# Kernel optimization log

Measured on AMD Instinct MI355X. Metric: run time of the kernel, lower is better.

The kernel has to match this reference:

```python
import jax, jax.numpy as jnp
import numpy as np

B, D, H, L = 2048, 4096, 1024, 64
LAM = 1.0  # topo_lambda


def setup_inputs() -> dict:
    key = jax.random.key(0)
    ks = jax.random.split(key, 5)
    def w(k, sh):
        fan_in = sh[0]
        return (jax.random.normal(k, sh, jnp.float32) * (1.0 / fan_in) ** 0.5)
    return {
        "x": jax.random.normal(ks[0], (B, D), jnp.float32),
        "W1": w(ks[1], (D, H)), "b1": jnp.zeros((H,), jnp.float32),
        "W2": w(ks[2], (H, L)), "b2": jnp.zeros((L,), jnp.float32),
        "W3": w(ks[3], (L, H)), "b3": jnp.zeros((H,), jnp.float32),
        "W4": w(ks[4], (H, D)), "b4": jnp.zeros((D,), jnp.float32),
        "latent_norm": jnp.ones((1,), jnp.float32),
    }


def _cdist(a):
    # pairwise euclidean distances [N, N], safe sqrt (zero grad on zero diag)
    sq = jnp.sum(a * a, axis=1)
    d2 = jnp.maximum(sq[:, None] + sq[None, :] - 2.0 * (a @ a.T), 0.0)
    pos = d2 > 0
    return jnp.where(pos, jnp.sqrt(jnp.where(pos, d2, 1.0)), 0.0)


def _mst_edges(d):
    # 0-dim persistence pairs == MST edges of the dense distance matrix.
    # Vectorized Prim's algorithm: scan of N-1 steps, O(N) work per step.
    n = d.shape[0]
    in_tree = jnp.zeros((n,), bool).at[0].set(True)
    min_dist = d[0]
    parent = jnp.zeros((n,), jnp.int32)

    def step(carry, _):
        in_tree, min_dist, parent = carry
        j = jnp.argmin(jnp.where(in_tree, jnp.inf, min_dist)).astype(jnp.int32)
        i = parent[j]
        in_tree = in_tree.at[j].set(True)
        better = (d[j] < min_dist) & ~in_tree
        min_dist = jnp.where(better, d[j], min_dist)
        parent = jnp.where(better, j, parent)
        return (in_tree, min_dist, parent), jnp.stack([i, j])

    _, edges = jax.lax.scan(step, (in_tree, min_dist, parent), None, length=n - 1)
    return edges  # [n-1, 2] int32


def _topo_signature(dx, dz):
    # pairing indices computed on detached distances (as in torch .detach())
    p1 = _mst_edges(jax.lax.stop_gradient(dx))
    p2 = _mst_edges(jax.lax.stop_gradient(dz))
    sig1 = dx[p1[:, 0], p1[:, 1]]
    sig1_2 = dz[p1[:, 0], p1[:, 1]]
    sig2 = dz[p2[:, 0], p2[:, 1]]
    sig2_1 = dx[p2[:, 0], p2[:, 1]]
    # match_edges == 'symmetric'
    return jnp.sum((sig1 - sig1_2) ** 2) + jnp.sum((sig2 - sig2_1) ** 2)


def reference(x, W1, b1, W2, b2, W3, b3, W4, b4, latent_norm):
    z = jax.nn.relu(x @ W1 + b1) @ W2 + b2            # [B, L]
    x_rec = jax.nn.relu(z @ W3 + b3) @ W4 + b4        # [B, D]
    rec_loss = jnp.mean((x_rec - x) ** 2)
    x_dist = _cdist(x)
    x_dist = x_dist / jnp.max(x_dist)
    z_dist = _cdist(z) / latent_norm[0]
    topo_loss = _topo_signature(x_dist, z_dist) / x.shape[0]
    loss = rec_loss + LAM * topo_loss
    return loss
```

## Files before the change

kernel.cpp:

```cpp
#include <hip/hip_runtime.h>
#include <hip/hip_bf16.h>

#define B_N 2048
#define D_N 4096
#define H_N 1024
#define L_N 64
#define NTILE 136
#define SPLK 4

typedef __attribute__((ext_vector_type(8))) short short8;
typedef __attribute__((ext_vector_type(4))) float float4_t;

#define ASG __attribute__((address_space(1)))
#define ASL __attribute__((address_space(3)))

__device__ inline float bf2f(unsigned short u) {
  union { unsigned u; float f; } v; v.u = ((unsigned)u) << 16; return v.f;
}
__device__ inline unsigned short f2bf(float f) {
  union { float f; unsigned u; } v; v.f = f;
  unsigned r = v.u + 0x7fffu + ((v.u >> 16) & 1u);
  return (unsigned short)(r >> 16);
}

__device__ inline float block_sum256(float v) {
  const int lane = threadIdx.x & 63, wave = threadIdx.x >> 6;
#pragma unroll
  for (int off = 32; off; off >>= 1) v += __shfl_xor(v, off);
  __shared__ float red_s[4];
  if (lane == 0) red_s[wave] = v;
  __syncthreads();
  return red_s[0] + red_s[1] + red_s[2] + red_s[3];
}

__device__ inline float block_max256(float v) {
  const int lane = threadIdx.x & 63, wave = threadIdx.x >> 6;
#pragma unroll
  for (int off = 32; off; off >>= 1) v = fmaxf(v, __shfl_xor(v, off));
  __shared__ float redm_s[4];
  if (lane == 0) redm_s[wave] = v;
  __syncthreads();
  return fmaxf(fmaxf(redm_s[0], redm_s[1]), fmaxf(redm_s[2], redm_s[3]));
}

__device__ inline void tri_idx(int b, int& tm, int& tn) {
  int m = (int)((sqrtf(8.f * (float)b + 1.f) - 1.f) * 0.5f);
  while ((m + 1) * (m + 2) / 2 <= b) ++m;
  while (m * (m + 1) / 2 > b) --m;
  tm = m;
  tn = b - m * (m + 1) / 2;
}

__global__ __launch_bounds__(256) void mega_prep(const float* __restrict__ x,
                                                 const float* __restrict__ W1,
                                                 const float* __restrict__ W4,
                                                 unsigned short* __restrict__ xb,
                                                 unsigned short* __restrict__ w1bt,
                                                 unsigned short* __restrict__ w4bt,
                                                 float* __restrict__ sqx,
                                                 float* __restrict__ accum,
                                                 int* __restrict__ comp,
                                                 unsigned long long* __restrict__ rowbest,
                                                 int* __restrict__ cnt,
                                                 int* __restrict__ done) {
  const int b = blockIdx.x;
  const int t = threadIdx.x;
  if (b < B_N) {
    const float4* xr = (const float4*)(x + (size_t)b * D_N);
    float s = 0.f;
    for (int i = t; i < D_N / 4; i += 256) {
      float4 v = xr[i];
      s += v.x * v.x + v.y * v.y + v.z * v.z + v.w * v.w;
      ushort4 o;
      o.x = f2bf(v.x); o.y = f2bf(v.y); o.z = f2bf(v.z); o.w = f2bf(v.w);
      const int p = i >> 3;
      const int k31 = (4 * i) & 31;
      *(ushort4*)(xb + ((size_t)p * B_N + b) * 32 + k31) = o;
    }
    float tot = block_sum256(s);
    if (t == 0) sqx[b] = tot;
    return;
  }
  if (b == B_N) {
    if (t < 2) { accum[t] = 0.f; cnt[t] = 0; done[t] = 0; }
    for (int v = t; v < 2 * B_N; v += 256) {
      comp[v] = v & (B_N - 1);
      rowbest[v] = ~0ull;
    }
    return;
  }
  int tb = b - (B_N + 1);
  const float* in;
  unsigned short* out;
  int C, bx, by;
  if (tb < 4096) { in = W1; out = w1bt; C = H_N; bx = tb & 31;  by = tb >> 5; }
  else { tb -= 4096; in = W4; out = w4bt; C = D_N; bx = tb & 127; by = tb >> 7; }
  const int c0 = bx * 32, r0 = by * 32;
  const int tx = t & 31, ty = t >> 5;
  __shared__ float tile[32][33];
#pragma unroll
  for (int i = 0; i < 32; i += 8)
    tile[ty + i][tx] = in[(size_t)(r0 + ty + i) * C + c0 + tx];
  __syncthreads();
#pragma unroll
  for (int i = 0; i < 32; i += 8)
    out[((size_t)(r0 >> 5) * C + c0 + ty + i) * 32 + tx] = f2bf(tile[tx][ty + i]);
}

__device__ inline void gemm_mainloop(const unsigned short* __restrict__ A,
                                     const unsigned short* __restrict__ Bt,
                                     int nrA, int nrB, int Klen, int m_base, int n_base,
                                     float4_t acc[4][4]) {
  __shared__ unsigned short lA[128 * 32];
  __shared__ unsigned short lB[128 * 32];
  const int t = threadIdx.x;
  const int wave = t >> 6;
  const int lane = t & 63;
  const int lrow = lane & 15;
  const int quad = lane >> 4;
  const int wm = (wave & 1) * 64;
  const int wn = (wave >> 1) * 64;
  const int srow = lane >> 2;
  const int scol = (lane & 3) * 8;

  for (int k0 = 0; k0 < Klen; k0 += 32) {
    const size_t pA = (size_t)(k0 >> 5) * nrA;
    const size_t pB = (size_t)(k0 >> 5) * nrB;
    __syncthreads();
#pragma unroll
    for (int q = 0; q < 2; ++q) {
      const int rbase = wave * 32 + q * 16;
      const int row = rbase + srow;
      __builtin_amdgcn_global_load_lds(
          (ASG void*)(A + (pA + m_base + row) * 32 + scol),
          (ASL void*)(lA + rbase * 32), 16, 0, 0);
      __builtin_amdgcn_global_load_lds(
          (ASG void*)(Bt + (pB + n_base + row) * 32 + scol),
          (ASL void*)(lB + rbase * 32), 16, 0, 0);
    }
    __syncthreads();
    short8 af[4], bfr[4];
#pragma unroll
    for (int f = 0; f < 4; ++f) {
      af[f]  = *(const short8*)(lA + (wm + f * 16 + lrow) * 32 + quad * 8);
      bfr[f] = *(const short8*)(lB + (wn + f * 16 + lrow) * 32 + quad * 8);
    }
#pragma unroll
    for (int fm = 0; fm < 4; ++fm)
#pragma unroll
      for (int fn = 0; fn < 4; ++fn)
        acc[fm][fn] = __builtin_amdgcn_mfma_f32_16x16x32_bf16(af[fm], bfr[fn],
                                                              acc[fm][fn], 0, 0, 0);
  }
}

__global__ __launch_bounds__(256) void mega_gemm(const unsigned short* __restrict__ xb,
                                                 const unsigned short* __restrict__ w1bt,
                                                 float* __restrict__ partsG1,
                                                 float* __restrict__ partsD2) {
  float4_t acc[4][4];
  float4_t z4 = {0.f, 0.f, 0.f, 0.f};
#pragma unroll
  for (int a = 0; a < 4; ++a)
#pragma unroll
    for (int b2 = 0; b2 < 4; ++b2) acc[a][b2] = z4;
  const int b = blockIdx.x;
  const int t = threadIdx.x, wave = t >> 6, lane = t & 63;
  const int lrow = lane & 15, quad = lane >> 4;
  const int wm = (wave & 1) * 64, wn = (wave >> 1) * 64;

  if (b < 512) {
    const int s = b >> 7;
    const int tt = b & 127;
    const int m_base = (tt >> 3) * 128, n_base = (tt & 7) * 128;
    const size_t po = (size_t)(s * 32);
    gemm_mainloop(xb + po * B_N * 32, w1bt + po * H_N * 32, B_N, H_N, D_N / SPLK,
                  m_base, n_base, acc);
    float* __restrict__ P = partsG1 + (size_t)s * B_N * H_N;
#pragma unroll
    for (int fm = 0; fm < 4; ++fm)
#pragma unroll
      for (int fn = 0; fn < 4; ++fn) {
        const int r0 = m_base + wm + fm * 16 + quad * 4;
        const int c = n_base + wn + fn * 16 + lrow;
#pragma unroll
        for (int r = 0; r < 4; ++r)
          P[(size_t)(r0 + r) * H_N + c] = acc[fm][fn][r];
      }
  } else {
    const int c = b - 512;
    const int s = c / NTILE;
    const int tt = c - s * NTILE;
    const int tile = (tt & 7) * 17 + (tt >> 3);
    int tm, tn;
    tri_idx(tile, tm, tn);
    const size_t po = (size_t)(s * 32) * B_N * 32;
    gemm_mainloop(xb + po, xb + po, B_N, B_N, D_N / SPLK, tm * 128, tn * 128, acc);
    float* __restrict__ P = partsD2 + ((size_t)s * NTILE + tile) * 16384;
#pragma unroll
    for (int fm = 0; fm < 4; ++fm)
#pragma unroll
      for (int fn = 0; fn < 4; ++fn) {
        const int lr0 = wm + fm * 16 + quad * 4;
        const int lc = wn + fn * 16 + lrow;
#pragma unroll
        for (int r = 0; r < 4; ++r)
          P[(lr0 + r) * 128 + lc] = acc[fm][fn][r];
      }
  }
}

__global__ __launch_bounds__(256) void mega_fin(const float* __restrict__ partsG1,
                                                const float* __restrict__ partsD2,
                                                const float* __restrict__ bias,
                                                const float* __restrict__ sq,
                                                unsigned short* __restrict__ h1b,
                                                float* __restrict__ d2x,
                                                unsigned* __restrict__ max_slot) {
  const int b = blockIdx.x;
  const int t = threadIdx.x;
  if (b < 2048) {
    const size_t MN = (size_t)B_N * H_N;
    const size_t i4 = ((size_t)b * 256 + t) * 4;
    float4 a = *(const float4*)(partsG1 + i4);
#pragma unroll
    for (int s = 1; s < SPLK; ++s) {
      float4 p = *(const float4*)(partsG1 + s * MN + i4);
      a.x += p.x; a.y += p.y; a.z += p.z; a.w += p.w;
    }
    const int row = (int)(i4 >> 10);
    const int k = (int)(i4 & (H_N - 1));
    float4 bb = *(const float4*)(bias + k);
    ushort4 o;
    o.x = f2bf(fmaxf(a.x + bb.x, 0.f));
    o.y = f2bf(fmaxf(a.y + bb.y, 0.f));
    o.z = f2bf(fmaxf(a.z + bb.z, 0.f));
    o.w = f2bf(fmaxf(a.w + bb.w, 0.f));
    *(ushort4*)(h1b + ((size_t)(k >> 5) * B_N + row) * 32 + (k & 31)) = o;
    return;
  }
  const int cidx = b - 2048;
  const int tile = cidx >> 2;
  const int c0 = (cidx & 3) * 32;
  int tm, tn;
  tri_idx(tile, tm, tn);
  __shared__ float lds[32][132];
  const int cc = (t & 7) * 4;
  float lmax = 0.f;
#pragma unroll
  for (int q = 0; q < 4; ++q) {
    const int r = (t >> 3) + 32 * q;
    const float* base = partsD2 + (size_t)tile * 16384 + r * 128 + c0 + cc;
    float4 a = *(const float4*)base;
#pragma unroll
    for (int s = 1; s < SPLK; ++s) {
      float4 p = *(const float4*)(base + (size_t)s * NTILE * 16384);
      a.x += p.x; a.y += p.y; a.z += p.z; a.w += p.w;
    }
    const int i = tm * 128 + r;
    const float si = sq[i];
    float4 sj = *(const float4*)(sq + tn * 128 + c0 + cc);
    float4 v;
    v.x = fmaxf(si + sj.x - 2.f * a.x, 0.f);
    v.y = fmaxf(si + sj.y - 2.f * a.y, 0.f);
    v.z = fmaxf(si + sj.z - 2.f * a.z, 0.f);
    v.w = fmaxf(si + sj.w - 2.f * a.w, 0.f);
    *(float4*)(d2x + (size_t)i * B_N + tn * 128 + c0 + cc) = v;
    lds[cc + 0][r] = v.x;
    lds[cc + 1][r] = v.y;
    lds[cc + 2][r] = v.z;
    lds[cc + 3][r] = v.w;
    lmax = fmaxf(lmax, fmaxf(fmaxf(v.x, v.y), fmaxf(v.z, v.w)));
  }
  __syncthreads();
#pragma unroll
  for (int m = 0; m < 4; ++m) {
    const int lin = t + 256 * m;
    const int cc2 = lin >> 5;
    const int r4 = (lin & 31) * 4;
    float4 w = *(const float4*)(&lds[cc2][r4]);
    *(float4*)(d2x + (size_t)(tn * 128 + c0 + cc2) * B_N + tm * 128 + r4) = w;
  }
  float tot = block_max256(lmax);
  if (t == 0) atomicMax(max_slot, __float_as_uint(tot));
}

__global__ __launch_bounds__(256) void g2_k(const unsigned short* __restrict__ h1b,
                                            const float* __restrict__ W2,
                                            const float* __restrict__ b2,
                                            float* __restrict__ z,
                                            float* __restrict__ sqz) {
  const int col = threadIdx.x & 63;
  const int row = blockIdx.x * 4 + (threadIdx.x >> 6);
  float a0 = 0.f, a1 = 0.f, a2 = 0.f, a3 = 0.f;
  for (int p = 0; p < H_N / 32; ++p) {
    const unsigned short* hb = h1b + ((size_t)p * B_N + row) * 32;
    const float* wb = W2 + (p * 32) * L_N + col;
#pragma unroll
    for (int k2 = 0; k2 < 32; k2 += 4) {
      a0 += bf2f(hb[k2 + 0]) * wb[(k2 + 0) * L_N];
      a1 += bf2f(hb[k2 + 1]) * wb[(k2 + 1) * L_N];
      a2 += bf2f(hb[k2 + 2]) * wb[(k2 + 2) * L_N];
      a3 += bf2f(hb[k2 + 3]) * wb[(k2 + 3) * L_N];
    }
  }
  const float zv = (a0 + a1) + (a2 + a3) + b2[col];
  z[(size_t)row * L_N + col] = zv;
  float s = zv * zv;
#pragma unroll
  for (int off = 32; off; off >>= 1) s += __shfl_xor(s, off);
  if (col == 0) sqz[row] = s;
}

__global__ __launch_bounds__(256) void mega_g3_d2z(const float* __restrict__ z,
                                                   const float* __restrict__ W3,
                                                   const float* __restrict__ b3,
                                                   const float* __restrict__ sqz,
                                                   unsigned short* __restrict__ h2b,
                                                   float* __restrict__ d2z) {
  const int b = blockIdx.x;
  const int t = threadIdx.x;
  if (b < 2048) {
    const int rg = b & 511, cg = b >> 9;
    const int col = cg * 256 + t;
    const int r0 = rg * 4;
    __shared__ float zr[4][64];
    zr[t >> 6][t & 63] = z[(size_t)(r0 + (t >> 6)) * L_N + (t & 63)];
    __syncthreads();
    const float bc = b3[col];
    float a0 = bc, a1 = bc, a2 = bc, a3 = bc;
#pragma unroll 8
    for (int k = 0; k < 64; ++k) {
      float w = W3[k * H_N + col];
      a0 += zr[0][k] * w;
      a1 += zr[1][k] * w;
      a2 += zr[2][k] * w;
      a3 += zr[3][k] * w;
    }
    const size_t base = ((size_t)(col >> 5) * B_N) * 32 + (col & 31);
    h2b[base + (size_t)(r0 + 0) * 32] = f2bf(fmaxf(a0, 0.f));
    h2b[base + (size_t)(r0 + 1) * 32] = f2bf(fmaxf(a1, 0.f));
    h2b[base + (size_t)(r0 + 2) * 32] = f2bf(fmaxf(a2, 0.f));
    h2b[base + (size_t)(r0 + 3) * 32] = f2bf(fmaxf(a3, 0.f));
    return;
  }
  const int c = b - 2048;
  const int bi = (c >> 7) * 16, bj = (c & 127) * 16;
  __shared__ float zi[16][65], zj[16][65];
  for (int idx = t; idx < 16 * 64; idx += 256) {
    const int r = idx >> 6, cc = idx & 63;
    zi[r][cc] = z[(size_t)(bi + r) * L_N + cc];
    zj[r][cc] = z[(size_t)(bj + r) * L_N + cc];
  }
  __syncthreads();
  const int ti = t >> 4, tj = t & 15;
  float dot = 0.f;
#pragma unroll 8
  for (int k = 0; k < 64; ++k) dot += zi[ti][k] * zj[tj][k];
  float v = fmaxf(sqz[bi + ti] + sqz[bj + tj] - 2.f * dot, 0.f);
  d2z[(size_t)(bi + ti) * B_N + bj + tj] = v;
}

__device__ inline void scan_row(const float* __restrict__ row, const int* __restrict__ cp,
                                int i, int ci, unsigned long long* __restrict__ dst) {
  const int t = threadIdx.x;
  const unsigned ibase = (unsigned)(i << 11);
  unsigned long long k = ~0ull;
#pragma unroll
  for (int m = 0; m < 2; ++m) {
    const int j4 = (t + m * 256) * 4;
    float4 dv = *(const float4*)(row + j4);
    int4 cj = *(const int4*)(cp + j4);
    if (cj.x != ci) {
      unsigned long long key = (((unsigned long long)__float_as_uint(dv.x)) << 32) | (ibase | (unsigned)(j4 + 0));
      k = key < k ? key : k;
    }
    if (cj.y != ci) {
      unsigned long long key = (((unsigned long long)__float_as_uint(dv.y)) << 32) | (ibase | (unsigned)(j4 + 1));
      k = key < k ? key : k;
    }
    if (cj.z != ci) {
      unsigned long long key = (((unsigned long long)__float_as_uint(dv.z)) << 32) | (ibase | (unsigned)(j4 + 2));
      k = key < k ? key : k;
    }
    if (cj.w != ci) {
      unsigned long long key = (((unsigned long long)__float_as_uint(dv.w)) << 32) | (ibase | (unsigned)(j4 + 3));
      k = key < k ? key : k;
    }
  }
  const int lane = t & 63, wave = t >> 6;
#pragma unroll
  for (int off = 32; off; off >>= 1) {
    unsigned long long o = __shfl_xor(k, off);
    k = o < k ? o : k;
  }
  __shared__ unsigned long long wmin[4];
  if (lane == 0) wmin[wave] = k;
  __syncthreads();
  if (t == 0) {
    unsigned long long a = wmin[0] < wmin[1] ? wmin[0] : wmin[1];
    unsigned long long b = wmin[2] < wmin[3] ? wmin[2] : wmin[3];
    *dst = (a < b) ? a : b;
  }
}

__global__ __launch_bounds__(256) void mega_recloss_scan0(
    const unsigned short* __restrict__ h2b, const unsigned short* __restrict__ w4bt,
    const float* __restrict__ bias, const float* __restrict__ Xref,
    float* __restrict__ acc_slot,
    const float* __restrict__ d2x, const float* __restrict__ d2z,
    const int* __restrict__ comp, unsigned long long* __restrict__ rowbest) {
  const int b = blockIdx.x;
  const int t = threadIdx.x;
  if (b < 512) {
    float4_t acc[4][4];
    float4_t z4 = {0.f, 0.f, 0.f, 0.f};
#pragma unroll
    for (int a = 0; a < 4; ++a)
#pragma unroll
      for (int b2 = 0; b2 < 4; ++b2) acc[a][b2] = z4;
    const int m_base = (b >> 5) * 128, n_base = (b & 31) * 128;
    gemm_mainloop(h2b, w4bt, B_N, D_N, H_N, m_base, n_base, acc);
    const int wave = t >> 6, lane = t & 63;
    const int lrow = lane & 15, quad = lane >> 4;
    const int wm = (wave & 1) * 64, wn = (wave >> 1) * 64;
    float local = 0.f;
#pragma unroll
    for (int fm = 0; fm < 4; ++fm)
#pragma unroll
      for (int fn = 0; fn < 4; ++fn) {
        const int r0 = m_base + wm + fm * 16 + quad * 4;
        const int c = n_base + wn + fn * 16 + lrow;
        const float bc = bias[c];
#pragma unroll
        for (int r = 0; r < 4; ++r) {
          float v = acc[fm][fn][r] + bc - Xref[(size_t)(r0 + r) * D_N + c];
          local += v * v;
        }
      }
    float tot = block_sum256(local);
    if (t == 0) atomicAdd(acc_slot, tot);
    return;
  }
  const int c = b - 512;
  const int i = c & (B_N - 1);
  const int tree = c >> 11;
  const float* __restrict__ d2 = tree ? d2z : d2x;
  const int* __restrict__ cp = comp + tree * B_N;
  scan_row(d2 + (size_t)i * B_N, cp, i, cp[i], rowbest + tree * B_N + i);
}

__global__ __launch_bounds__(256) void bor_scan(const float* __restrict__ d2x,
                                                const float* __restrict__ d2z,
                                                const int* __restrict__ comp,
                                                unsigned long long* __restrict__ rowbest,
                                                const int* __restrict__ done) {
  const int tree = blockIdx.y;
  if (done[tree]) return;
  const int i = blockIdx.x;
  const int* __restrict__ cp = comp + tree * B_N;
  const int ci = cp[i];
  const unsigned long long prev = rowbest[tree * B_N + i];
  if (prev != ~0ull) {
    const int j = (int)(prev & (unsigned)(B_N - 1));
    if (cp[j] != ci) return;
  }
  const float* __restrict__ d2 = tree ? d2z : d2x;
  scan_row(d2 + (size_t)i * B_N, cp, i, ci, rowbest + tree * B_N + i);
}

__global__ __launch_bounds__(1024) void bor_merge(const unsigned long long* __restrict__ rowbest,
                                                  int* __restrict__ comp,
                                                  int2* __restrict__ edges,
                                                  int* __restrict__ cnt,
                                                  int* __restrict__ done) {
  const int tree = blockIdx.x;
  if (done[tree]) return;
  const unsigned long long* __restrict__ rb = rowbest + tree * B_N;
  int* __restrict__ cp = comp + tree * B_N;
  int2* __restrict__ eo = edges + (size_t)tree * (B_N - 1);
  int* __restrict__ cn = cnt + tree;
  __shared__ unsigned long long bc[B_N];
  __shared__ int hk[B_N];
  __shared__ int allsame;
  const int t = threadIdx.x;

#pragma unroll
  for (int q = 0; q < 2; ++q) bc[t + q * 1024] = ~0ull;
  __syncthreads();
#pragma unroll
  for (int q = 0; q < 2; ++q) {
    const int i = t + q * 1024;
    const unsigned long long key = rb[i];
    if (key != ~0ull) atomicMin(&bc[cp[i]], key);
  }
  __syncthreads();

  unsigned long long mykey[2];
#pragma unroll
  for (int q = 0; q < 2; ++q) {
    const int c = t + q * 1024;
    const unsigned long long key = bc[c];
    mykey[q] = key;
    int h = c;
    if (key != ~0ull) h = cp[(unsigned)key & (unsigned)(B_N - 1)];
    hk[c] = h;
  }
  __syncthreads();

  int rloc[2];
#pragma unroll
  for (int q = 0; q < 2; ++q) {
    const int c = t + q * 1024;
    const unsigned long long key = mykey[q];
    const int h = hk[c];
    const int hh = hk[h];
    const bool valid = key != ~0ull;
    const bool two = (h != c) && (hh == c);
    rloc[q] = (two && c < h) ? c : h;
    if (valid && (!two || c < h)) {
      int e = atomicAdd(cn, 1);
      eo[e] = make_int2((int)((key >> 11) & (unsigned)(B_N - 1)),
                        (int)(key & (unsigned)(B_N - 1)));
    }
  }
  __syncthreads();
#pragma unroll
  for (int q = 0; q < 2; ++q) hk[t + q * 1024] = rloc[q];
  if (t == 0) allsame = 1;
  __syncthreads();

  for (int it = 0; it < 11; ++it) {
    const int v0 = hk[hk[t]];
    const int v1 = hk[hk[t + 1024]];
    __syncthreads();
    hk[t] = v0;
    hk[t + 1024] = v1;
    __syncthreads();
  }

#pragma unroll
  for (int q = 0; q < 2; ++q) {
    const int v = t + q * 1024;
    cp[v] = hk[cp[v]];
  }
  __syncthreads();
  const int c0v = cp[0];
  if (cp[t] != c0v || cp[t + 1024] != c0v) allsame = 0;
  __syncthreads();
  if (t == 0 && allsame) done[tree] = 1;
}

__global__ __launch_bounds__(256) void final_k(const float* __restrict__ d2x,
                                               const float* __restrict__ d2z,
                                               const int2* __restrict__ edges,
                                               const float* __restrict__ accum,
                                               const float* __restrict__ latent_norm,
                                               float* __restrict__ out) {
  const int t = threadIdx.x;
  const float maxd = sqrtf(__uint_as_float(((const unsigned*)accum)[1]));
  const float inv_maxd = 1.0f / maxd;
  const float inv_ln = 1.0f / latent_norm[0];
  float local = 0.f;
  for (int e = t; e < 2 * (B_N - 1); e += 256) {
    int2 ij = edges[e];
    size_t idx = (size_t)ij.x * B_N + ij.y;
    float xd = sqrtf(d2x[idx]) * inv_maxd;
    float zd = sqrtf(d2z[idx]) * inv_ln;
    float d = xd - zd;
    local += d * d;
  }
  float topo = block_sum256(local);
  if (t == 0)
    out[0] = accum[0] * (1.0f / ((float)B_N * (float)D_N)) + topo * (1.0f / (float)B_N);
}

extern "C" void kernel_launch(void* const* d_in, const int* in_sizes, int n_in,
                              void* d_out, int out_size, void* d_ws, size_t ws_size,
                              hipStream_t stream) {
  const float* x  = (const float*)d_in[0];
  const float* W1 = (const float*)d_in[1];
  const float* b1 = (const float*)d_in[2];
  const float* W2 = (const float*)d_in[3];
  const float* b2 = (const float*)d_in[4];
  const float* W3 = (const float*)d_in[5];
  const float* b3 = (const float*)d_in[6];
  const float* W4 = (const float*)d_in[7];
  const float* b4 = (const float*)d_in[8];
  const float* latent_norm = (const float*)d_in[9];
  float* out = (float*)d_out;

  char* ws = (char*)d_ws;
  size_t off = 0;
  auto alloc = [&](size_t bytes) {
    size_t o = off;
    off += (bytes + 255) & ~(size_t)255;
    return o;
  };
  unsigned short* xb   = (unsigned short*)(ws + alloc((size_t)B_N * D_N * 2));
  unsigned short* w1bt = (unsigned short*)(ws + alloc((size_t)H_N * D_N * 2));
  unsigned short* w4bt = (unsigned short*)(ws + alloc((size_t)D_N * H_N * 2));
  unsigned short* h1b  = (unsigned short*)(ws + alloc((size_t)B_N * H_N * 2));
  unsigned short* h2b  = (unsigned short*)(ws + alloc((size_t)B_N * H_N * 2));
  float* z    = (float*)(ws + alloc((size_t)B_N * L_N * 4));
  float* sqx  = (float*)(ws + alloc((size_t)B_N * 4));
  float* sqz  = (float*)(ws + alloc((size_t)B_N * 4));
  float* d2x  = (float*)(ws + alloc((size_t)B_N * B_N * 4));
  float* d2z  = (float*)(ws + alloc((size_t)B_N * B_N * 4));
  int2* edges = (int2*)(ws + alloc((size_t)2 * (B_N - 1) * sizeof(int2)));
  float* accum = (float*)(ws + alloc(256));
  int* comp   = (int*)(ws + alloc((size_t)2 * B_N * 4));
  unsigned long long* rowbest = (unsigned long long*)(ws + alloc((size_t)2 * B_N * 8));
  int* cnt    = (int*)(ws + alloc(256));
  int* done   = (int*)(ws + alloc(256));
  float* partsG1 = (float*)(ws + alloc((size_t)SPLK * B_N * H_N * 4));
  float* partsD2 = (float*)(ws + alloc((size_t)SPLK * NTILE * 16384 * 4));

  mega_prep<<<B_N + 1 + 8192, 256, 0, stream>>>(x, W1, W4, xb, w1bt, w4bt, sqx,
                                                accum, comp, rowbest, cnt, done);
  mega_gemm<<<512 + SPLK * NTILE, 256, 0, stream>>>(xb, w1bt, partsG1, partsD2);
  mega_fin<<<2048 + 4 * NTILE, 256, 0, stream>>>(partsG1, partsD2, b1, sqx, h1b, d2x,
                                                 (unsigned*)(accum + 1));
  g2_k<<<B_N / 4, 256, 0, stream>>>(h1b, W2, b2, z, sqz);
  mega_g3_d2z<<<2048 + 16384, 256, 0, stream>>>(z, W3, b3, sqz, h2b, d2z);
  mega_recloss_scan0<<<512 + 2 * B_N, 256, 0, stream>>>(h2b, w4bt, b4, x, accum,
                                                        d2x, d2z, comp, rowbest);
  bor_merge<<<2, 1024, 0, stream>>>(rowbest, comp, edges, cnt, done);
  for (int r = 1; r < 11; ++r) {
    bor_scan<<<dim3(B_N, 2), 256, 0, stream>>>(d2x, d2z, comp, rowbest, done);
    bor_merge<<<2, 1024, 0, stream>>>(rowbest, comp, edges, cnt, done);
  }
  final_k<<<1, 256, 0, stream>>>(d2x, d2z, edges, accum, latent_norm, out);
}
```

Measured before the change: 407.0 us.

## Fuse Boruvka merge into scan kernel with redundant per-block merge and ping-pong buffers

```diff
diff --git a/kernel.cpp b/kernel.cpp
--- a/kernel.cpp
+++ b/kernel.cpp
@@ -450,105 +450,152 @@
   scan_row(d2 + (size_t)i * B_N, cp, i, cp[i], rowbest + tree * B_N + i);
 }
 
-__global__ __launch_bounds__(256) void bor_scan(const float* __restrict__ d2x,
-                                                const float* __restrict__ d2z,
-                                                const int* __restrict__ comp,
-                                                unsigned long long* __restrict__ rowbest,
-                                                const int* __restrict__ done) {
-  const int tree = blockIdx.y;
+__global__ __launch_bounds__(256) void bor_round_f(
+    const float* __restrict__ d2x, const float* __restrict__ d2z,
+    const int* __restrict__ comp_old, int* __restrict__ comp_new,
+    const unsigned long long* __restrict__ rb_old, unsigned long long* __restrict__ rb_new,
+    int2* __restrict__ edges, int* __restrict__ cnt, int* __restrict__ done,
+    int do_scan) {
+  const int blk = blockIdx.x;
+  const int tree = blk >> 11;
+  const int i = blk & (B_N - 1);
   if (done[tree]) return;
-  const int i = blockIdx.x;
-  const int* __restrict__ cp = comp + tree * B_N;
-  const int ci = cp[i];
-  const unsigned long long prev = rowbest[tree * B_N + i];
-  if (prev != ~0ull) {
-    const int j = (int)(prev & (unsigned)(B_N - 1));
-    if (cp[j] != ci) return;
-  }
-  const float* __restrict__ d2 = tree ? d2z : d2x;
-  scan_row(d2 + (size_t)i * B_N, cp, i, ci, rowbest + tree * B_N + i);
-}
-
-__global__ __launch_bounds__(1024) void bor_merge(const unsigned long long* __restrict__ rowbest,
-                                                  int* __restrict__ comp,
-                                                  int2* __restrict__ edges,
-                                                  int* __restrict__ cnt,
-                                                  int* __restrict__ done) {
-  const int tree = blockIdx.x;
-  if (done[tree]) return;
-  const unsigned long long* __restrict__ rb = rowbest + tree * B_N;
-  int* __restrict__ cp = comp + tree * B_N;
+  const int t = threadIdx.x;
+  const bool desig = (i == 0);
+
+  const int* __restrict__ co_g = comp_old + tree * B_N;
+  int* __restrict__ cn_g = comp_new + tree * B_N;
+  const unsigned long long* __restrict__ ro_g = rb_old + tree * B_N;
+  unsigned long long* __restrict__ rn_g = rb_new + tree * B_N;
   int2* __restrict__ eo = edges + (size_t)tree * (B_N - 1);
-  int* __restrict__ cn = cnt + tree;
+  int* __restrict__ cn_cnt = cnt + tree;
+
+  __shared__ int co[B_N];
   __shared__ unsigned long long bc[B_N];
   __shared__ int hk[B_N];
   __shared__ int allsame;
-  const int t = threadIdx.x;
-
-#pragma unroll
-  for (int q = 0; q < 2; ++q) bc[t + q * 1024] = ~0ull;
-  __syncthreads();
-#pragma unroll
-  for (int q = 0; q < 2; ++q) {
-    const int i = t + q * 1024;
-    const unsigned long long key = rb[i];
-    if (key != ~0ull) atomicMin(&bc[cp[i]], key);
-  }
-  __syncthreads();
-
-  unsigned long long mykey[2];
-#pragma unroll
-  for (int q = 0; q < 2; ++q) {
-    const int c = t + q * 1024;
+
+#pragma unroll
+  for (int q = 0; q < 8; ++q) {
+    const int v = t + 256 * q;
+    co[v] = co_g[v];
+    bc[v] = ~0ull;
+  }
+  __syncthreads();
+
+#pragma unroll
+  for (int q = 0; q < 8; ++q) {
+    const int v = t + 256 * q;
+    const unsigned long long key = ro_g[v];
+    if (key != ~0ull) atomicMin(&bc[co[v]], key);
+  }
+  __syncthreads();
+
+  unsigned long long mykey[8];
+#pragma unroll
+  for (int q = 0; q < 8; ++q) {
+    const int c = t + 256 * q;
     const unsigned long long key = bc[c];
     mykey[q] = key;
     int h = c;
-    if (key != ~0ull) h = cp[(unsigned)key & (unsigned)(B_N - 1)];
+    if (key != ~0ull) h = co[(unsigned)key & (unsigned)(B_N - 1)];
     hk[c] = h;
   }
   __syncthreads();
 
-  int rloc[2];
-#pragma unroll
-  for (int q = 0; q < 2; ++q) {
-    const int c = t + q * 1024;
+  int rloc[8];
+#pragma unroll
+  for (int q = 0; q < 8; ++q) {
+    const int c = t + 256 * q;
     const unsigned long long key = mykey[q];
     const int h = hk[c];
     const int hh = hk[h];
     const bool valid = key != ~0ull;
     const bool two = (h != c) && (hh == c);
     rloc[q] = (two && c < h) ? c : h;
-    if (valid && (!two || c < h)) {
-      int e = atomicAdd(cn, 1);
+    if (desig && valid && (!two || c < h)) {
+      int e = atomicAdd(cn_cnt, 1);
       eo[e] = make_int2((int)((key >> 11) & (unsigned)(B_N - 1)),
                         (int)(key & (unsigned)(B_N - 1)));
     }
   }
   __syncthreads();
 #pragma unroll
-  for (int q = 0; q < 2; ++q) hk[t + q * 1024] = rloc[q];
+  for (int q = 0; q < 8; ++q) hk[t + 256 * q] = rloc[q];
   if (t == 0) allsame = 1;
   __syncthreads();
 
   for (int it = 0; it < 11; ++it) {
-    const int v0 = hk[hk[t]];
-    const int v1 = hk[hk[t + 1024]];
+    int v[8];
+#pragma unroll
+    for (int q = 0; q < 8; ++q) v[q] = hk[hk[t + 256 * q]];
     __syncthreads();
-    hk[t] = v0;
-    hk[t + 1024] = v1;
+#pragma unroll
+    for (int q = 0; q < 8; ++q) hk[t + 256 * q] = v[q];
     __syncthreads();
   }
 
-#pragma unroll
-  for (int q = 0; q < 2; ++q) {
-    const int v = t + q * 1024;
-    cp[v] = hk[cp[v]];
-  }
-  __syncthreads();
-  const int c0v = cp[0];
-  if (cp[t] != c0v || cp[t + 1024] != c0v) allsame = 0;
-  __syncthreads();
-  if (t == 0 && allsame) done[tree] = 1;
+  const int c0v = hk[co[0]];
+#pragma unroll
+  for (int q = 0; q < 8; ++q)
+    if (hk[co[t + 256 * q]] != c0v) allsame = 0;
+  __syncthreads();
+  if (desig) {
+#pragma unroll
+    for (int q = 0; q < 8; ++q) {
+      const int v = t + 256 * q;
+      cn_g[v] = hk[co[v]];
+    }
+    if (t == 0 && allsame) done[tree] = 1;
+  }
+  if (allsame || !do_scan) return;
+
+  const int ci = hk[co[i]];
+  const unsigned long long prev = ro_g[i];
+  if (prev != ~0ull) {
+    const int j = (int)(prev & (unsigned)(B_N - 1));
+    if (hk[co[j]] != ci) {
+      if (t == 0) rn_g[i] = prev;
+      return;
+    }
+  }
+  const float* __restrict__ row = (tree ? d2z : d2x) + (size_t)i * B_N;
+  const unsigned ibase = (unsigned)(i << 11);
+  unsigned long long k = ~0ull;
+#pragma unroll
+  for (int m = 0; m < 2; ++m) {
+    const int j4 = (t + m * 256) * 4;
+    float4 dv = *(const float4*)(row + j4);
+    if (hk[co[j4 + 0]] != ci) {
+      unsigned long long key = (((unsigned long long)__float_as_uint(dv.x)) << 32) | (ibase | (unsigned)(j4 + 0));
+      k = key < k ? key : k;
+    }
+    if (hk[co[j4 + 1]] != ci) {
+      unsigned long long key = (((unsigned long long)__float_as_uint(dv.y)) << 32) | (ibase | (unsigned)(j4 + 1));
+      k = key < k ? key : k;
+    }
+    if (hk[co[j4 + 2]] != ci) {
+      unsigned long long key = (((unsigned long long)__float_as_uint(dv.z)) << 32) | (ibase | (unsigned)(j4 + 2));
+      k = key < k ? key : k;
+    }
+    if (hk[co[j4 + 3]] != ci) {
+      unsigned long long key = (((unsigned long long)__float_as_uint(dv.w)) << 32) | (ibase | (unsigned)(j4 + 3));
+      k = key < k ? key : k;
+    }
+  }
+  const int lane = t & 63, wave = t >> 6;
+#pragma unroll
+  for (int off = 32; off; off >>= 1) {
+    unsigned long long o = __shfl_xor(k, off);
+    k = o < k ? o : k;
+  }
+  if (lane == 0) bc[wave] = k;
+  __syncthreads();
+  if (t == 0) {
+    unsigned long long a = bc[0] < bc[1] ? bc[0] : bc[1];
+    unsigned long long b2 = bc[2] < bc[3] ? bc[2] : bc[3];
+    rn_g[i] = (a < b2) ? a : b2;
+  }
 }
 
 __global__ __launch_bounds__(256) void final_k(const float* __restrict__ d2x,
@@ -609,26 +656,31 @@
   float* d2z  = (float*)(ws + alloc((size_t)B_N * B_N * 4));
   int2* edges = (int2*)(ws + alloc((size_t)2 * (B_N - 1) * sizeof(int2)));
   float* accum = (float*)(ws + alloc(256));
-  int* comp   = (int*)(ws + alloc((size_t)2 * B_N * 4));
-  unsigned long long* rowbest = (unsigned long long*)(ws + alloc((size_t)2 * B_N * 8));
+  int* compA  = (int*)(ws + alloc((size_t)2 * B_N * 4));
+  int* compB  = (int*)(ws + alloc((size_t)2 * B_N * 4));
+  unsigned long long* rbA = (unsigned long long*)(ws + alloc((size_t)2 * B_N * 8));
+  unsigned long long* rbB = (unsigned long long*)(ws + alloc((size_t)2 * B_N * 8));
   int* cnt    = (int*)(ws + alloc(256));
   int* done   = (int*)(ws + alloc(256));
   float* partsG1 = (float*)(ws + alloc((size_t)SPLK * B_N * H_N * 4));
   float* partsD2 = (float*)(ws + alloc((size_t)SPLK * NTILE * 16384 * 4));
 
   mega_prep<<<B_N + 1 + 8192, 256, 0, stream>>>(x, W1, W4, xb, w1bt, w4bt, sqx,
-                                                accum, comp, rowbest, cnt, done);
+                                                accum, compA, rbA, cnt, done);
   mega_gemm<<<512 + SPLK * NTILE, 256, 0, stream>>>(xb, w1bt, partsG1, partsD2);
   mega_fin<<<2048 + 4 * NTILE, 256, 0, stream>>>(partsG1, partsD2, b1, sqx, h1b, d2x,
                                                  (unsigned*)(accum + 1));
   g2_k<<<B_N / 4, 256, 0, stream>>>(h1b, W2, b2, z, sqz);
   mega_g3_d2z<<<2048 + 16384, 256, 0, stream>>>(z, W3, b3, sqz, h2b, d2z);
   mega_recloss_scan0<<<512 + 2 * B_N, 256, 0, stream>>>(h2b, w4bt, b4, x, accum,
-                                                        d2x, d2z, comp, rowbest);
-  bor_merge<<<2, 1024, 0, stream>>>(rowbest, comp, edges, cnt, done);
-  for (int r = 1; r < 11; ++r) {
-    bor_scan<<<dim3(B_N, 2), 256, 0, stream>>>(d2x, d2z, comp, rowbest, done);
-    bor_merge<<<2, 1024, 0, stream>>>(rowbest, comp, edges, cnt, done);
+                                                        d2x, d2z, compA, rbA);
+  for (int r = 1; r <= 11; ++r) {
+    const int* co = (r & 1) ? compA : compB;
+    int* cn_ = (r & 1) ? compB : compA;
+    const unsigned long long* ro = (r & 1) ? rbA : rbB;
+    unsigned long long* rn = (r & 1) ? rbB : rbA;
+    bor_round_f<<<2 * B_N, 256, 0, stream>>>(d2x, d2z, co, cn_, ro, rn,
+                                             edges, cnt, done, (r < 11) ? 1 : 0);
   }
   final_k<<<1, 256, 0, stream>>>(d2x, d2z, edges, accum, latent_norm, out);
 }
```

Result: slower. 506.5 us (+24.5%).
